# Performance work log

Hardware: AMD Instinct MI355X
Metric: run time of the kernel (lower is better)

The kernel has to match this reference:

```python
import jax, jax.numpy as jnp
import numpy as np

N, E, F_IN, H1, H2, C, G = 100000, 1600000, 128, 128, 64, 10, 64

def setup_inputs() -> dict:
    key = jax.random.key(0)
    ks = jax.random.split(key, 10)
    x = jax.random.normal(ks[0], (N, F_IN), dtype=jnp.float32)
    edge_index = jax.random.randint(ks[1], (2, E), 0, N, dtype=jnp.int32)
    batch = jnp.sort(jax.random.randint(ks[2], (N,), 0, G, dtype=jnp.int32))
    W1 = jax.random.normal(ks[3], (F_IN, H1), dtype=jnp.float32) * 0.05
    b1 = jnp.zeros((H1,), dtype=jnp.float32)
    W2 = jax.random.normal(ks[4], (H1, H2), dtype=jnp.float32) * 0.05
    b2 = jnp.zeros((H2,), dtype=jnp.float32)
    Wfc = jax.random.normal(ks[5], (H2, C), dtype=jnp.float32) * 0.05
    bfc = jnp.zeros((C,), dtype=jnp.float32)
    return {"x": x, "edge_index": edge_index, "batch": batch,
            "W1": W1, "b1": b1, "W2": W2, "b2": b2, "Wfc": Wfc, "bfc": bfc}

def gcn_conv(x, src, dst, W, b, n_nodes):
    # PyG GCNConv: add self-loops, symmetric normalization D^-1/2 A D^-1/2, linear, bias
    h = x @ W  # [N, H]
    deg = jnp.zeros((n_nodes,), h.dtype).at[dst].add(1.0) + 1.0  # +1 self-loop
    dinv = jax.lax.rsqrt(deg)
    norm = dinv[src] * dinv[dst]  # [E]
    msg = h[src] * norm[:, None]  # gather + scale
    agg = jnp.zeros_like(h).at[dst].add(msg)  # scatter-add at target
    agg = agg + h * (dinv * dinv)[:, None]    # self-loop messages
    return agg + b

def global_mean_pool(x, batch, num_graphs):
    sums = jnp.zeros((num_graphs, x.shape[1]), x.dtype).at[batch].add(x)
    cnt = jnp.zeros((num_graphs,), x.dtype).at[batch].add(1.0)
    return sums / jnp.maximum(cnt, 1.0)[:, None]

def reference(x, edge_index, batch, W1, b1, W2, b2, Wfc, bfc):
    src, dst = edge_index[0], edge_index[1]
    h = gcn_conv(x, src, dst, W1, b1, N)
    h = jax.nn.relu(h)
    # dropout is identity in eval mode
    h = gcn_conv(h, src, dst, W2, b2, N)
    g = global_mean_pool(h, batch, G)  # [G, 64]
    return g @ Wfc + bfc  # [G, C]
```

## Files before the change

kernel.cpp:

```cpp
#include <hip/hip_runtime.h>
#include <cstdint>

#define NN   100000
#define NE   1600000
#define FIN  128
#define HH1  128
#define HH2  64
#define NC   10
#define NG   64

#define NB   256
#define NPB  392
#define BCAP 8192
#define EPS  4096
#define NBLK_B ((NE + EPS - 1) / EPS)

typedef __attribute__((ext_vector_type(8))) short bf16x8;
typedef __attribute__((ext_vector_type(4))) float f32x4;
typedef __attribute__((ext_vector_type(2))) float f32x2;

#if defined(__has_builtin)
#  if __has_builtin(__builtin_amdgcn_cvt_pk_f32_fp8) && \
      __has_builtin(__builtin_amdgcn_cvt_f32_fp8) && \
      __has_builtin(__builtin_amdgcn_cvt_pk_fp8_f32)
#    define HW_FP8 1
#  endif
#endif
#ifndef HW_FP8
#  define HW_FP8 0
#endif

__device__ __forceinline__ unsigned pack2(float a, float b) {
    union { float f; unsigned u; } x, y; x.f = a; y.f = b;
    const unsigned lo = x.u + 0x7fffu + ((x.u >> 16) & 1u);
    const unsigned hi = y.u + 0x7fffu + ((y.u >> 16) & 1u);
    return (lo >> 16) | (hi & 0xffff0000u);
}

__device__ __forceinline__ float sw_dec8(unsigned b) {
    const unsigned s = b >> 7, e = (b >> 3) & 15u, m = b & 7u;
    float v;
    if (e == 0) v = (float)m * 0.001953125f;
    else { union { unsigned u; float f; } y; y.u = ((e + 120u) << 23) | (m << 20); v = y.f; }
    return s ? -v : v;
}
__device__ __forceinline__ unsigned sw_enc8(float f) {
    union { float f; unsigned u; } x; x.f = f;
    const unsigned s = (x.u >> 31) << 7;
    float a = fabsf(f);
    a = fminf(a, 448.0f);
    unsigned ia;
    if (a < 0.015625f) {
        ia = (unsigned)(int)rintf(a * 512.0f);
    } else {
        union { float f; unsigned u; } y; y.f = a;
        int e = (int)((y.u >> 23) & 255u) - 127;
        unsigned keep = (y.u >> 20) & 7u;
        const unsigned rest = y.u & 0xfffffu;
        keep += (rest > 0x80000u) || (rest == 0x80000u && (keep & 1u));
        if (keep == 8u) { keep = 0u; e += 1; }
        if (e >= 8) { e = 8; if (keep > 6u) keep = 6u; }
        ia = ((unsigned)(e + 7) << 3) | keep;
    }
    return s | ia;
}
__device__ __forceinline__ f32x4 fp8x4_f32(unsigned u) {
#if HW_FP8
    f32x2 lo = __builtin_amdgcn_cvt_pk_f32_fp8(u, false);
    f32x2 hi = __builtin_amdgcn_cvt_pk_f32_fp8(u, true);
    return (f32x4){lo[0], lo[1], hi[0], hi[1]};
#else
    return (f32x4){sw_dec8(u & 0xffu), sw_dec8((u >> 8) & 0xffu),
                   sw_dec8((u >> 16) & 0xffu), sw_dec8(u >> 24)};
#endif
}
__device__ __forceinline__ float fp8_f32(unsigned b) {
#if HW_FP8
    return __builtin_amdgcn_cvt_f32_fp8(b, 0);
#else
    return sw_dec8(b & 0xffu);
#endif
}
__device__ __forceinline__ unsigned f32_fp8(float a) {
#if HW_FP8
    return __builtin_amdgcn_cvt_pk_fp8_f32(a, a, 0u, false) & 0xffu;
#else
    return sw_enc8(a);
#endif
}
__device__ __forceinline__ unsigned pack4_fp8(float a, float b, float c, float d) {
#if HW_FP8
    unsigned u = __builtin_amdgcn_cvt_pk_fp8_f32(a, b, 0u, false);
    u = __builtin_amdgcn_cvt_pk_fp8_f32(c, d, u, true);
    return u;
#else
    return sw_enc8(a) | (sw_enc8(b) << 8) | (sw_enc8(c) << 16) | (sw_enc8(d) << 24);
#endif
}

__global__ __launch_bounds__(256) void k_init(int* __restrict__ gcursor,
                                              float* __restrict__ sums) {
    const int i = blockIdx.x * blockDim.x + threadIdx.x;
    if (i < NB) gcursor[i] = i * BCAP;
    if (i < NG * HH2 + NG) sums[i] = 0.f;
}

__global__ __launch_bounds__(256) void k_bscatter(const int* __restrict__ src,
                                                  const int* __restrict__ dst,
                                                  int* __restrict__ gcursor,
                                                  unsigned* __restrict__ pairs, int E) {
    __shared__ int cnt[NB];
    __shared__ int lst[NB];
    __shared__ int bglob[NB];
    __shared__ unsigned buf[EPS];
    __shared__ int gd[EPS];
    const int t = threadIdx.x;
    cnt[t] = 0;
    __syncthreads();
    const int base = blockIdx.x * EPS;
    unsigned val[16]; int bo[16];
#pragma unroll
    for (int i = 0; i < 4; ++i) {
        const int e = base + i * 1024 + t * 4;
        if (e < E) {
            const int4 d = *(const int4*)&dst[e];
            const int4 s = *(const int4*)&src[e];
            unsigned bk;
            bk = (unsigned)d.x / NPB;
            val[i * 4 + 0] = ((unsigned)s.x << 9) | ((unsigned)d.x - bk * NPB);
            bo[i * 4 + 0] = (int)((bk << 16) | (unsigned)atomicAdd(&cnt[bk], 1));
            bk = (unsigned)d.y / NPB;
            val[i * 4 + 1] = ((unsigned)s.y << 9) | ((unsigned)d.y - bk * NPB);
            bo[i * 4 + 1] = (int)((bk << 16) | (unsigned)atomicAdd(&cnt[bk], 1));
            bk = (unsigned)d.z / NPB;
            val[i * 4 + 2] = ((unsigned)s.z << 9) | ((unsigned)d.z - bk * NPB);
            bo[i * 4 + 2] = (int)((bk << 16) | (unsigned)atomicAdd(&cnt[bk], 1));
            bk = (unsigned)d.w / NPB;
            val[i * 4 + 3] = ((unsigned)s.w << 9) | ((unsigned)d.w - bk * NPB);
            bo[i * 4 + 3] = (int)((bk << 16) | (unsigned)atomicAdd(&cnt[bk], 1));
        } else {
            bo[i * 4 + 0] = bo[i * 4 + 1] = bo[i * 4 + 2] = bo[i * 4 + 3] = -1;
        }
    }
    __syncthreads();
    const int v = cnt[t];
    lst[t] = v;
    __syncthreads();
    for (int off = 1; off < 256; off <<= 1) {
        const int x = (t >= off) ? lst[t - off] : 0;
        __syncthreads();
        lst[t] += x;
        __syncthreads();
    }
    const int total = lst[NB - 1];
    const int excl = lst[t] - v;
    if (v > 0) bglob[t] = atomicAdd(&gcursor[t], v);
    __syncthreads();
    lst[t] = excl;
    __syncthreads();
#pragma unroll
    for (int i = 0; i < 16; ++i) {
        if (bo[i] >= 0) {
            const int bk = bo[i] >> 16;
            const int r  = bo[i] & 0xffff;
            const int pos = lst[bk] + r;
            buf[pos] = val[i];
            gd[pos]  = bglob[bk] + r;
        }
    }
    __syncthreads();
    for (int p = t; p < total; p += 256)
        pairs[gd[p]] = buf[p];
}

__global__ __launch_bounds__(512) void k_csr(const unsigned* __restrict__ pairs,
                                             const int* __restrict__ gcursor,
                                             int* __restrict__ row_start,
                                             int* __restrict__ rend,
                                             float* __restrict__ dinv,
                                             int* __restrict__ esrc) {
    const int b = blockIdx.x;
    const int node0 = b * NPB;
    if (node0 >= NN) return;
    const int nn = min(NPB, NN - node0);
    __shared__ int cnt[NPB];
    __shared__ int scn[512];
    __shared__ int cur[NPB];
    const int t = threadIdx.x;
    if (t < NPB) cnt[t] = 0;
    __syncthreads();
    const int ebeg = b * BCAP, eend = gcursor[b];
    for (int j = ebeg + t; j < eend; j += 512)
        atomicAdd(&cnt[pairs[j] & 511u], 1);
    __syncthreads();
    const int v = (t < nn) ? cnt[t] : 0;
    const int pv = (v + 3) & ~3;
    scn[t] = pv;
    __syncthreads();
    for (int off = 1; off < 512; off <<= 1) {
        const int x = (t >= off) ? scn[t - off] : 0;
        __syncthreads();
        scn[t] += x;
        __syncthreads();
    }
    if (t < nn) {
        const int rs = ebeg + scn[t] - pv;
        row_start[node0 + t] = rs;
        rend[node0 + t]      = rs + v;
        cur[t] = rs;
        dinv[node0 + t] = rsqrtf((float)v + 1.f);
    }
    __syncthreads();
    for (int j = ebeg + t; j < eend; j += 512) {
        const unsigned p = pairs[j];
        const int pos = atomicAdd(&cur[p & 511u], 1);
        esrc[pos] = (int)(p >> 9);
    }
}

template <int BN, bool ABF16>
__global__ __launch_bounds__(256) void k_mfma(const void* __restrict__ Ain,
                                              const float* __restrict__ Bin,
                                              unsigned char* __restrict__ Cout,
                                              const float* __restrict__ rowscale,
                                              int M) {
    __shared__ unsigned short Bs[BN][128];
    const int t = threadIdx.x;
    const int row0 = blockIdx.x * 128;

    {
        constexpr int KSEG = (BN == 128) ? 64 : 32;
        const int n  = t & (BN - 1);
        const int kb = (t / BN) * KSEG;
#pragma unroll
        for (int i = 0; i < KSEG; i += 2) {
            const int k = kb + i;
            const unsigned u = pack2(Bin[(size_t)k * BN + n], Bin[(size_t)(k + 1) * BN + n]);
            *(unsigned*)&Bs[n][(((k >> 3) ^ (n & 7)) << 3) + (k & 7)] = u;
        }
    }

    const int lane = t & 63, wave = t >> 6;
    const int lr = lane & 15, lg = lane >> 4;
    constexpr int MR = 2;
    constexpr int NR = BN / 16;
    const int wrow = wave * 32;

    bf16x8 afrag[4][MR];
#pragma unroll
    for (int m = 0; m < MR; ++m) {
        int row = row0 + wrow + m * 16 + lr;
        row = (row < M) ? row : (M - 1);
        if (ABF16) {
            const uint4* ap = (const uint4*)((const unsigned short*)Ain + (size_t)row * 128);
#pragma unroll
            for (int ks = 0; ks < 4; ++ks) {
                const uint4 v = ap[ks * 4 + lg];
                afrag[ks][m] = *(const bf16x8*)&v;
            }
        } else {
            const float* ap = (const float*)Ain + (size_t)row * 128;
#pragma unroll
            for (int ks = 0; ks < 4; ++ks) {
                const float4 f0 = *(const float4*)(ap + ks * 32 + lg * 8);
                const float4 f1 = *(const float4*)(ap + ks * 32 + lg * 8 + 4);
                const uint4 v = make_uint4(pack2(f0.x, f0.y), pack2(f0.z, f0.w),
                                           pack2(f1.x, f1.y), pack2(f1.z, f1.w));
                afrag[ks][m] = *(const bf16x8*)&v;
            }
        }
    }
    __syncthreads();

    f32x4 acc[MR][NR];
#pragma unroll
    for (int m = 0; m < MR; ++m)
#pragma unroll
        for (int n = 0; n < NR; ++n) acc[m][n] = (f32x4){0.f, 0.f, 0.f, 0.f};

#pragma unroll
    for (int ks = 0; ks < 4; ++ks) {
        const int cc = ((ks * 4 + lg) ^ (lr & 7)) * 8;
        bf16x8 b[NR];
#pragma unroll
        for (int n = 0; n < NR; ++n) b[n] = *(const bf16x8*)&Bs[n * 16 + lr][cc];
#pragma unroll
        for (int m = 0; m < MR; ++m)
#pragma unroll
            for (int n = 0; n < NR; ++n)
                acc[m][n] = __builtin_amdgcn_mfma_f32_16x16x32_bf16(afrag[ks][m], b[n], acc[m][n], 0, 0, 0);
    }

#pragma unroll
    for (int m = 0; m < MR; ++m) {
        const int rb = wrow + m * 16 + lg * 4;
        float s[4]; int gr[4];
#pragma unroll
        for (int j = 0; j < 4; ++j) {
            gr[j] = row0 + rb + j;
            s[j] = (gr[j] < M) ? rowscale[gr[j]] : 0.f;
        }
#pragma unroll
        for (int n = 0; n < NR; ++n) {
            const int col = n * 16 + lr;
#pragma unroll
            for (int j = 0; j < 4; ++j)
                if (gr[j] < M)
                    Cout[(size_t)gr[j] * BN + col] = (unsigned char)f32_fp8(acc[m][n][j] * s[j]);
        }
    }
}

__global__ __launch_bounds__(256) void k_agg1(const int* __restrict__ row_start,
                                              const int* __restrict__ row_end,
                                              const int* __restrict__ esrc,
                                              const float* __restrict__ dinv,
                                              const uint2* __restrict__ hb,
                                              const float* __restrict__ b,
                                              uint4* __restrict__ outp, int n) {
    const int wid  = (blockIdx.x * blockDim.x + threadIdx.x) >> 6;
    const int lane = threadIdx.x & 63;
    if (wid >= n) return;
    const int q  = lane >> 4;
    const int ql = lane & 15;
    const int beg = row_start[wid], end = row_end[wid];

    f32x4 accA = (f32x4){0.f, 0.f, 0.f, 0.f};
    f32x4 accB = accA;
    if (q == 0) {
        const uint2 u = hb[(size_t)wid * 16 + ql];
        accA = fp8x4_f32(u.x);
        accB = fp8x4_f32(u.y);
    }

    int j = beg;
    for (; j + 16 <= end; j += 16) {
        const int4 ix = *(const int4*)&esrc[j + q * 4];
        const uint2 u0 = hb[(size_t)ix.x * 16 + ql];
        const uint2 u1 = hb[(size_t)ix.y * 16 + ql];
        const uint2 u2 = hb[(size_t)ix.z * 16 + ql];
        const uint2 u3 = hb[(size_t)ix.w * 16 + ql];
        accA += (fp8x4_f32(u0.x) + fp8x4_f32(u1.x)) + (fp8x4_f32(u2.x) + fp8x4_f32(u3.x));
        accB += (fp8x4_f32(u0.y) + fp8x4_f32(u1.y)) + (fp8x4_f32(u2.y) + fp8x4_f32(u3.y));
    }
    for (; j + 4 <= end; j += 4) {
        const uint2 u = hb[(size_t)esrc[j + q] * 16 + ql];
        accA += fp8x4_f32(u.x);
        accB += fp8x4_f32(u.y);
    }
    if (j + q < end) {
        const uint2 u = hb[(size_t)esrc[j + q] * 16 + ql];
        accA += fp8x4_f32(u.x);
        accB += fp8x4_f32(u.y);
    }

#pragma unroll
    for (int k = 0; k < 4; ++k) {
        accA[k] += __shfl_xor(accA[k], 16); accA[k] += __shfl_xor(accA[k], 32);
        accB[k] += __shfl_xor(accB[k], 16); accB[k] += __shfl_xor(accB[k], 32);
    }

    if (q == 0) {
        const float dd = dinv[wid];
        const float4 bv0 = *(const float4*)&b[ql * 8];
        const float4 bv1 = *(const float4*)&b[ql * 8 + 4];
        float r[8];
        r[0] = fmaxf(fmaf(dd, accA[0], bv0.x), 0.f);
        r[1] = fmaxf(fmaf(dd, accA[1], bv0.y), 0.f);
        r[2] = fmaxf(fmaf(dd, accA[2], bv0.z), 0.f);
        r[3] = fmaxf(fmaf(dd, accA[3], bv0.w), 0.f);
        r[4] = fmaxf(fmaf(dd, accB[0], bv1.x), 0.f);
        r[5] = fmaxf(fmaf(dd, accB[1], bv1.y), 0.f);
        r[6] = fmaxf(fmaf(dd, accB[2], bv1.z), 0.f);
        r[7] = fmaxf(fmaf(dd, accB[3], bv1.w), 0.f);
        outp[(size_t)wid * 16 + ql] = make_uint4(pack2(r[0], r[1]), pack2(r[2], r[3]),
                                                 pack2(r[4], r[5]), pack2(r[6], r[7]));
    }
}

__global__ __launch_bounds__(256) void k_agg2(const int* __restrict__ row_start,
                                              const int* __restrict__ row_end,
                                              const int* __restrict__ esrc,
                                              const float* __restrict__ dinv,
                                              const uint2* __restrict__ hb,
                                              const float* __restrict__ b,
                                              uint2* __restrict__ outp, int n) {
    const int wid  = (blockIdx.x * blockDim.x + threadIdx.x) >> 6;
    const int lane = threadIdx.x & 63;
    if (wid >= n) return;
    const int o  = lane >> 3;
    const int ol = lane & 7;
    const int beg = row_start[wid], end = row_end[wid];

    f32x4 accA = (f32x4){0.f, 0.f, 0.f, 0.f};
    f32x4 accB = accA;
    if (o == 0) {
        const uint2 u = hb[(size_t)wid * 8 + ol];
        accA = fp8x4_f32(u.x);
        accB = fp8x4_f32(u.y);
    }

    int j = beg;
    for (; j + 16 <= end; j += 16) {
        const int2 ix = *(const int2*)&esrc[j + o * 2];
        const uint2 u0 = hb[(size_t)ix.x * 8 + ol];
        const uint2 u1 = hb[(size_t)ix.y * 8 + ol];
        accA += fp8x4_f32(u0.x) + fp8x4_f32(u1.x);
        accB += fp8x4_f32(u0.y) + fp8x4_f32(u1.y);
    }
    for (; j + 8 <= end; j += 8) {
        const uint2 u = hb[(size_t)esrc[j + o] * 8 + ol];
        accA += fp8x4_f32(u.x);
        accB += fp8x4_f32(u.y);
    }
    if (j + o < end) {
        const uint2 u = hb[(size_t)esrc[j + o] * 8 + ol];
        accA += fp8x4_f32(u.x);
        accB += fp8x4_f32(u.y);
    }

#pragma unroll
    for (int k = 0; k < 4; ++k) {
        accA[k] += __shfl_xor(accA[k], 8);
        accA[k] += __shfl_xor(accA[k], 16);
        accA[k] += __shfl_xor(accA[k], 32);
        accB[k] += __shfl_xor(accB[k], 8);
        accB[k] += __shfl_xor(accB[k], 16);
        accB[k] += __shfl_xor(accB[k], 32);
    }

    if (o == 0) {
        const float dd = dinv[wid];
        const float4 bv0 = *(const float4*)&b[ol * 8];
        const float4 bv1 = *(const float4*)&b[ol * 8 + 4];
        const unsigned w0 = pack4_fp8(fmaf(dd, accA[0], bv0.x), fmaf(dd, accA[1], bv0.y),
                                      fmaf(dd, accA[2], bv0.z), fmaf(dd, accA[3], bv0.w));
        const unsigned w1 = pack4_fp8(fmaf(dd, accB[0], bv1.x), fmaf(dd, accB[1], bv1.y),
                                      fmaf(dd, accB[2], bv1.z), fmaf(dd, accB[3], bv1.w));
        outp[(size_t)wid * 8 + ol] = make_uint2(w0, w1);
    }
}

__global__ __launch_bounds__(256) void k_pool(const unsigned char* __restrict__ v2,
                                              const int* __restrict__ batch,
                                              float* __restrict__ sums,
                                              float* __restrict__ cnt, int n) {
    constexpr int NPW = 128;
    const int gt = blockIdx.x * blockDim.x + threadIdx.x;
    const int wave = gt >> 6;
    const int lane = threadIdx.x & 63;
    const int start = wave * NPW;
    if (start >= n) return;
    const int end = min(start + NPW, n);
    float acc = 0.f, cacc = 0.f;
    int cur = batch[start];
    for (int nd = start; nd < end; ++nd) {
        const int gid = batch[nd];
        if (gid != cur) {
            atomicAdd(&sums[cur * HH2 + lane], acc);
            if (lane == 0) atomicAdd(&cnt[cur], cacc);
            acc = 0.f; cacc = 0.f; cur = gid;
        }
        acc += fp8_f32(v2[(size_t)nd * 64 + lane]);
        cacc += 1.f;
    }
    atomicAdd(&sums[cur * HH2 + lane], acc);
    if (lane == 0) atomicAdd(&cnt[cur], cacc);
}

__global__ void k_fc(const float* __restrict__ sums, const float* __restrict__ cnt,
                     const float* __restrict__ Wfc, const float* __restrict__ bfc,
                     float* __restrict__ out) {
    const int tid = threadIdx.x;
    if (tid >= NG * NC) return;
    const int g = tid / NC;
    const int c = tid % NC;
    float a = 0.f;
    for (int k = 0; k < HH2; ++k)
        a = fmaf(sums[g * HH2 + k], Wfc[k * NC + c], a);
    const float cg = fmaxf(cnt[g], 1.0f);
    out[g * NC + c] = a / cg + bfc[c];
}

extern "C" void kernel_launch(void* const* d_in, const int* in_sizes, int n_in,
                              void* d_out, int out_size, void* d_ws, size_t ws_size,
                              hipStream_t stream) {
    const float* x   = (const float*)d_in[0];
    const int*   ei  = (const int*)d_in[1];
    const int*   bat = (const int*)d_in[2];
    const float* W1  = (const float*)d_in[3];
    const float* b1  = (const float*)d_in[4];
    const float* W2  = (const float*)d_in[5];
    const float* b2  = (const float*)d_in[6];
    const float* Wfc = (const float*)d_in[7];
    const float* bfc = (const float*)d_in[8];
    float* out = (float*)d_out;

    const int* src = ei;
    const int* dst = ei + NE;

    float* ws = (float*)d_ws;
    unsigned* relu1     = (unsigned*)ws;
    unsigned char* v2   = (unsigned char*)ws;
    unsigned char* h1b  = (unsigned char*)(ws + (size_t)NN * 64);
    unsigned char* h2b  = (unsigned char*)(ws + (size_t)NN * 64);
    float*    dinv      = ws + (size_t)NN * 96;
    int*      row_start = (int*)(ws + (size_t)NN * 97);
    int*      rend      = (int*)(ws + (size_t)NN * 98);
    int*      esrc      = (int*)(ws + (size_t)NN * 99);
    unsigned* pairs     = (unsigned*)(ws + (size_t)NN * 99 + (size_t)NB * BCAP);
    float*    sums      = ws + (size_t)NN * 99 + 2 * (size_t)NB * BCAP;
    float*    cntf      = sums + NG * HH2;
    int*      gcursor   = (int*)(cntf + NG);

    k_init<<<(NG * HH2 + NG + 255) / 256, 256, 0, stream>>>(gcursor, sums);
    k_bscatter<<<NBLK_B, 256, 0, stream>>>(src, dst, gcursor, pairs, NE);
    k_csr<<<NB, 512, 0, stream>>>(pairs, gcursor, row_start, rend, dinv, esrc);

    const int gblk = (NN + 127) / 128;

    k_mfma<128, false><<<gblk, 256, 0, stream>>>(x, W1, h1b, dinv, NN);
    k_agg1<<<(NN * 64 + 255) / 256, 256, 0, stream>>>(row_start, rend, esrc, dinv,
                                                      (const uint2*)h1b, b1,
                                                      (uint4*)relu1, NN);

    k_mfma<64, true><<<gblk, 256, 0, stream>>>(relu1, W2, h2b, dinv, NN);
    k_agg2<<<(NN * 64 + 255) / 256, 256, 0, stream>>>(row_start, rend, esrc, dinv,
                                                      (const uint2*)h2b, b2,
                                                      (uint2*)v2, NN);

    {
        const int waves = (NN + 127) / 128;
        const int blocks = (waves * 64 + 255) / 256;
        k_pool<<<blocks, 256, 0, stream>>>(v2, bat, sums, cntf, NN);
    }

    k_fc<<<1, 640, 0, stream>>>(sums, cntf, Wfc, bfc, out);
}
```

Measured before the change: 221.4 us.

## Fuse second aggregation with mean pooling via per-node atomics; binary-search graph counts

Merges the layer-2 aggregation and the pooling kernel into one. Each node's wave now atomically adds its bias-adjusted features straight into the per-graph sums, so the FP8 intermediate node features are never written or read back and one launch goes away. Per-graph node counts are now found by binary search over the sorted batch array inside the init kernel. The cost is far more global float atomics (one per node-feature) aimed at only a few thousand addresses, which can contend heavily.

```diff
diff --git a/kernel.cpp b/kernel.cpp
--- a/kernel.cpp
+++ b/kernel.cpp
@@ -74,13 +74,6 @@
                    sw_dec8((u >> 16) & 0xffu), sw_dec8(u >> 24)};
 #endif
 }
-__device__ __forceinline__ float fp8_f32(unsigned b) {
-#if HW_FP8
-    return __builtin_amdgcn_cvt_f32_fp8(b, 0);
-#else
-    return sw_dec8(b & 0xffu);
-#endif
-}
 __device__ __forceinline__ unsigned f32_fp8(float a) {
 #if HW_FP8
     return __builtin_amdgcn_cvt_pk_fp8_f32(a, a, 0u, false) & 0xffu;
@@ -88,21 +81,23 @@
     return sw_enc8(a);
 #endif
 }
-__device__ __forceinline__ unsigned pack4_fp8(float a, float b, float c, float d) {
-#if HW_FP8
-    unsigned u = __builtin_amdgcn_cvt_pk_fp8_f32(a, b, 0u, false);
-    u = __builtin_amdgcn_cvt_pk_fp8_f32(c, d, u, true);
-    return u;
-#else
-    return sw_enc8(a) | (sw_enc8(b) << 8) | (sw_enc8(c) << 16) | (sw_enc8(d) << 24);
-#endif
-}
 
 __global__ __launch_bounds__(256) void k_init(int* __restrict__ gcursor,
-                                              float* __restrict__ sums) {
+                                              float* __restrict__ sums,
+                                              const int* __restrict__ bat,
+                                              float* __restrict__ cntf) {
     const int i = blockIdx.x * blockDim.x + threadIdx.x;
     if (i < NB) gcursor[i] = i * BCAP;
-    if (i < NG * HH2 + NG) sums[i] = 0.f;
+    if (i < NG * HH2) sums[i] = 0.f;
+    if (blockIdx.x == 0 && threadIdx.x < NG) {
+        const int g = threadIdx.x;
+        int lo = 0, hi = NN;
+        while (lo < hi) { const int m = (lo + hi) >> 1; if (bat[m] < g) lo = m + 1; else hi = m; }
+        const int lb = lo;
+        lo = 0; hi = NN;
+        while (lo < hi) { const int m = (lo + hi) >> 1; if (bat[m] < g + 1) lo = m + 1; else hi = m; }
+        cntf[g] = (float)(lo - lb);
+    }
 }
 
 __global__ __launch_bounds__(256) void k_bscatter(const int* __restrict__ src,
@@ -378,13 +373,14 @@
     }
 }
 
-__global__ __launch_bounds__(256) void k_agg2(const int* __restrict__ row_start,
-                                              const int* __restrict__ row_end,
-                                              const int* __restrict__ esrc,
-                                              const float* __restrict__ dinv,
-                                              const uint2* __restrict__ hb,
-                                              const float* __restrict__ b,
-                                              uint2* __restrict__ outp, int n) {
+__global__ __launch_bounds__(256) void k_agg2pool(const int* __restrict__ row_start,
+                                                  const int* __restrict__ row_end,
+                                                  const int* __restrict__ esrc,
+                                                  const float* __restrict__ dinv,
+                                                  const uint2* __restrict__ hb,
+                                                  const float* __restrict__ b,
+                                                  const int* __restrict__ bat,
+                                                  float* __restrict__ sums, int n) {
     const int wid  = (blockIdx.x * blockDim.x + threadIdx.x) >> 6;
     const int lane = threadIdx.x & 63;
     if (wid >= n) return;
@@ -429,43 +425,17 @@
         accB[k] += __shfl_xor(accB[k], 32);
     }
 
-    if (o == 0) {
-        const float dd = dinv[wid];
-        const float4 bv0 = *(const float4*)&b[ol * 8];
-        const float4 bv1 = *(const float4*)&b[ol * 8 + 4];
-        const unsigned w0 = pack4_fp8(fmaf(dd, accA[0], bv0.x), fmaf(dd, accA[1], bv0.y),
-                                      fmaf(dd, accA[2], bv0.z), fmaf(dd, accA[3], bv0.w));
-        const unsigned w1 = pack4_fp8(fmaf(dd, accB[0], bv1.x), fmaf(dd, accB[1], bv1.y),
-                                      fmaf(dd, accB[2], bv1.z), fmaf(dd, accB[3], bv1.w));
-        outp[(size_t)wid * 8 + ol] = make_uint2(w0, w1);
-    }
-}
-
-__global__ __launch_bounds__(256) void k_pool(const unsigned char* __restrict__ v2,
-                                              const int* __restrict__ batch,
-                                              float* __restrict__ sums,
-                                              float* __restrict__ cnt, int n) {
-    constexpr int NPW = 128;
-    const int gt = blockIdx.x * blockDim.x + threadIdx.x;
-    const int wave = gt >> 6;
-    const int lane = threadIdx.x & 63;
-    const int start = wave * NPW;
-    if (start >= n) return;
-    const int end = min(start + NPW, n);
-    float acc = 0.f, cacc = 0.f;
-    int cur = batch[start];
-    for (int nd = start; nd < end; ++nd) {
-        const int gid = batch[nd];
-        if (gid != cur) {
-            atomicAdd(&sums[cur * HH2 + lane], acc);
-            if (lane == 0) atomicAdd(&cnt[cur], cacc);
-            acc = 0.f; cacc = 0.f; cur = gid;
-        }
-        acc += fp8_f32(v2[(size_t)nd * 64 + lane]);
-        cacc += 1.f;
-    }
-    atomicAdd(&sums[cur * HH2 + lane], acc);
-    if (lane == 0) atomicAdd(&cnt[cur], cacc);
+    const float s0 = (o < 4) ? accA[0] : accB[0];
+    const float s1 = (o < 4) ? accA[1] : accB[1];
+    const float s2 = (o < 4) ? accA[2] : accB[2];
+    const float s3 = (o < 4) ? accA[3] : accB[3];
+    const int oo = o & 3;
+    const float val = (oo == 0) ? s0 : (oo == 1) ? s1 : (oo == 2) ? s2 : s3;
+
+    const int feat = ol * 8 + o;
+    const float dd = dinv[wid];
+    const int g = bat[wid];
+    atomicAdd(&sums[g * HH2 + feat], fmaf(dd, val, b[feat]));
 }
 
 __global__ void k_fc(const float* __restrict__ sums, const float* __restrict__ cnt,
@@ -501,7 +471,6 @@
 
     float* ws = (float*)d_ws;
     unsigned* relu1     = (unsigned*)ws;
-    unsigned char* v2   = (unsigned char*)ws;
     unsigned char* h1b  = (unsigned char*)(ws + (size_t)NN * 64);
     unsigned char* h2b  = (unsigned char*)(ws + (size_t)NN * 64);
     float*    dinv      = ws + (size_t)NN * 96;
@@ -513,7 +482,7 @@
     float*    cntf      = sums + NG * HH2;
     int*      gcursor   = (int*)(cntf + NG);
 
-    k_init<<<(NG * HH2 + NG + 255) / 256, 256, 0, stream>>>(gcursor, sums);
+    k_init<<<(NG * HH2 + 255) / 256, 256, 0, stream>>>(gcursor, sums, bat, cntf);
     k_bscatter<<<NBLK_B, 256, 0, stream>>>(src, dst, gcursor, pairs, NE);
     k_csr<<<NB, 512, 0, stream>>>(pairs, gcursor, row_start, rend, dinv, esrc);
 
@@ -525,15 +494,9 @@
                                                       (uint4*)relu1, NN);
 
     k_mfma<64, true><<<gblk, 256, 0, stream>>>(relu1, W2, h2b, dinv, NN);
-    k_agg2<<<(NN * 64 + 255) / 256, 256, 0, stream>>>(row_start, rend, esrc, dinv,
-                                                      (const uint2*)h2b, b2,
-                                                      (uint2*)v2, NN);
-
-    {
-        const int waves = (NN + 127) / 128;
-        const int blocks = (waves * 64 + 255) / 256;
-        k_pool<<<blocks, 256, 0, stream>>>(v2, bat, sums, cntf, NN);
-    }
+    k_agg2pool<<<(NN * 64 + 255) / 256, 256, 0, stream>>>(row_start, rend, esrc, dinv,
+                                                          (const uint2*)h2b, b2,
+                                                          bat, sums, NN);
 
     k_fc<<<1, 640, 0, stream>>>(sums, cntf, Wfc, bfc, out);
 }
```

Result: slower. 281.5 us (+27.2%).
